# Performance work log

Measured on AMD Instinct MI355X. Metric: run time of the kernel, lower is better.

## Reference

```python
import jax, jax.numpy as jnp
import numpy as np

DIM = 512
HEADS = 8
DIM_HEAD = 64  # default dim_head used for scale, matches DIM//HEADS here
SCALE = DIM_HEAD ** -0.5
B, X, Y = 8, 32, 32


def setup_inputs() -> dict:
    key = jax.random.key(0)
    k0, k1, k2, k3 = jax.random.split(key, 4)
    fmap = jax.random.normal(k0, (B, DIM, X, Y), dtype=jnp.float32)
    # 1x1 convs as matrices: weight [out, in]
    Wqkvl = jax.random.normal(k1, (4 * DIM, DIM), dtype=jnp.float32) * (DIM ** -0.5)
    Wout = jax.random.normal(k2, (DIM, DIM), dtype=jnp.float32) * (DIM ** -0.5)
    bout = jax.random.normal(k3, (DIM,), dtype=jnp.float32) * 0.01
    return {"fmap": fmap, "Wqkvl": Wqkvl, "Wout": Wout, "bout": bout}


def reference(fmap, Wqkvl, Wout, bout):
    b, c, x, y = fmap.shape
    h, d = HEADS, c // HEADS
    n = x * y
    # 1x1 conv projection to q,k,v,L
    qkvL = jnp.einsum('oc,bcxy->boxy', Wqkvl, fmap)  # [b, 4c, x, y]
    q, k, v, L = jnp.split(qkvL, 4, axis=1)
    # 'b (h d) x y -> b h (x y) d'
    def to_tokens(t):
        return t.reshape(b, h, d, n).transpose(0, 1, 3, 2)
    q, k, v, L = map(to_tokens, (q, k, v, L))
    dots = jnp.einsum('bhid,bhjd->bhij', q, k) * SCALE  # [b,h,n,n]
    attn = jax.nn.softmax(dots, axis=-1)
    out = jnp.einsum('bhij,bhjd->bhid', attn, v) + L  # [b,h,n,d]
    # 'b h (x y) d -> b (h d) x y'
    out = out.transpose(0, 1, 3, 2).reshape(b, c, x, y)
    # output 1x1 conv with bias (dropout=0 -> identity)
    out = jnp.einsum('oc,bcxy->boxy', Wout, out) + bout[None, :, None, None]
    return out
```

## Files before the change

### kernel.cpp

```cpp
#include <hip/hip_runtime.h>

#define Bn 8
#define Cn 512
#define Hn 8
#define Dn 64
#define Nn 1024
#define SCALEQ 0.18033688011112042f

typedef unsigned short u16;
typedef unsigned int u32;
typedef unsigned short u16x8 __attribute__((ext_vector_type(8)));
typedef unsigned short u16x4 __attribute__((ext_vector_type(4)));
typedef unsigned int u32x2 __attribute__((ext_vector_type(2)));
typedef short s16x4 __attribute__((ext_vector_type(4)));
typedef float f32x4 __attribute__((ext_vector_type(4)));
typedef __bf16 bf16x8 __attribute__((ext_vector_type(8)));

__device__ __forceinline__ u16 f2bf(float f){
  unsigned u = __float_as_uint(f);
  u += 0x7fffu + ((u >> 16) & 1u);
  return (u16)(u >> 16);
}
__device__ __forceinline__ float bf2f(u16 h){
  return __uint_as_float(((unsigned)h) << 16);
}
__device__ __forceinline__ f32x4 mfma16(u16x8 a, u16x8 b, f32x4 c){
  return __builtin_amdgcn_mfma_f32_16x16x32_bf16(
      __builtin_bit_cast(bf16x8, a), __builtin_bit_cast(bf16x8, b), c, 0, 0, 0);
}
__device__ __forceinline__ f32x4 mfma16k16(u16x4 a, u32x2 b, f32x4 c){
  return __builtin_amdgcn_mfma_f32_16x16x16bf16_1k(
      __builtin_bit_cast(s16x4, a), __builtin_bit_cast(s16x4, b), c, 0, 0, 0);
}
__device__ __forceinline__ float fexp2(float x){ return __builtin_amdgcn_exp2f(x); }
__device__ __forceinline__ u32 cvtpk(float a, float b){
  u32 r;
  asm("v_cvt_pk_bf16_f32 %0, %1, %2" : "=v"(r) : "v"(a), "v"(b));
  return r;
}

__device__ __forceinline__ void gload16(const u16* src, u16* dst){
  __builtin_amdgcn_global_load_lds(
      (const __attribute__((address_space(1))) unsigned int*)src,
      (__attribute__((address_space(3))) unsigned int*)dst, 16, 0, 0);
}

#define TILE_SYNC(N) do {                                     \
    asm volatile("s_waitcnt vmcnt(" #N ")" ::: "memory");     \
    __builtin_amdgcn_sched_barrier(0);                        \
    __builtin_amdgcn_s_barrier();                             \
    __builtin_amdgcn_sched_barrier(0);                        \
  } while(0)

__global__ __launch_bounds__(256) void k_prep(const float* __restrict__ fmap,
                                              u16* __restrict__ fmapT,
                                              const float* __restrict__ Wqkvl,
                                              const float* __restrict__ Wout,
                                              u16* __restrict__ W1bf, u16* __restrict__ Wobf){
  __shared__ float tile[64][33];
  const int bid = blockIdx.x;
  if (bid < 2048){
    const int n0 = (bid & 31) * 32, c0 = ((bid >> 5) & 7) * 64, b = bid >> 8;
    const int tx = threadIdx.x & 31, ty = threadIdx.x >> 5;
    const float* src = fmap + ((size_t)b * Cn + c0) * Nn + n0;
#pragma unroll
    for (int i = 0; i < 8; i++) tile[ty + 8*i][tx] = src[(size_t)(ty + 8*i) * Nn + tx];
    __syncthreads();
    const int nr = threadIdx.x >> 3;
    const int cj = (threadIdx.x & 7) * 8;
    u16x8 o;
#pragma unroll
    for (int k = 0; k < 8; k++) o[k] = f2bf(tile[cj + k][nr]);
    *reinterpret_cast<u16x8*>(fmapT + ((size_t)b * Nn + n0 + nr) * Cn + c0 + cj) = o;
  } else {
    const int n1 = Cn*Cn, n2 = Cn*Cn/4;
    int i = (bid - 2048) * 256 + threadIdx.x;
    const float* s; u16* d; int j;
    if (i < n1){ s = Wqkvl; d = W1bf; j = i; }
    else { if (i >= n1 + n2) return; s = Wout; d = Wobf; j = i - n1; }
    float4 f = reinterpret_cast<const float4*>(s)[j];
    u16x4 o;
    o[0] = f2bf(f.x); o[1] = f2bf(f.y); o[2] = f2bf(f.z); o[3] = f2bf(f.w);
    reinterpret_cast<u16x4*>(d)[j] = o;
  }
}

__device__ __forceinline__ void stage64(const u16* g, size_t ldg, u16* lbase, int w, int lane){
#pragma unroll
  for (int s = 0; s < 2; s++){
    int row = s*32 + w*8 + (lane>>3);
    gload16(g + (size_t)row*ldg + (((lane&7) ^ (row&7)) * 8), lbase + (s*32 + w*8)*64);
  }
}
__device__ __forceinline__ void stage128x32(const u16* g, size_t ldg, u16* lbase, int w, int lane){
#pragma unroll
  for (int s = 0; s < 2; s++){
    int row = s*64 + w*16 + (lane>>2);
    gload16(g + (size_t)row*ldg + (((lane&3) ^ (row&3)) * 8), lbase + (s*64 + w*16)*32);
  }
}
__device__ __forceinline__ void stage64x32(const u16* g, size_t ldg, u16* lbase, int w, int lane){
  int row = w*16 + (lane>>2);
  gload16(g + (size_t)row*ldg + (((lane&3) ^ (row&3)) * 8), lbase + (w*16)*32);
}

__device__ __forceinline__ void gemm_nt_128(const u16* __restrict__ Ap, int lda,
                                            const u16* __restrict__ Bp, int ldb,
                                            u16* sA, u16* sB,
                                            f32x4 (&acc)[4][4]){
  const int tid = threadIdx.x;
  const int w = tid >> 6, lane = tid & 63, r = lane & 15, g = lane >> 4;
  const int wi = w >> 1, wj = w & 1;
  stage128x32(Ap,      lda, sA,        w, lane);
  stage128x32(Bp,      ldb, sB,        w, lane);
  stage128x32(Ap + 32, lda, sA + 4096, w, lane);
  stage128x32(Bp + 32, ldb, sB + 4096, w, lane);
  int cur = 0;
  for (int ks = 0; ks < 16; ks++){
    if (ks < 15) TILE_SYNC(4);
    else         TILE_SYNC(0);
    if (ks + 2 < 16){
      int nxt = cur + 2; if (nxt >= 3) nxt -= 3;
      stage128x32(Ap + (ks+2)*32, lda, sA + nxt*4096, w, lane);
      stage128x32(Bp + (ks+2)*32, ldb, sB + nxt*4096, w, lane);
    }
    const u16* Al = sA + cur*4096;
    const u16* Bl = sB + cur*4096;
    u16x8 af[4], bf[4];
#pragma unroll
    for (int t = 0; t < 4; t++){
      int ar = wi*64 + t*16 + r;
      af[t] = *reinterpret_cast<const u16x8*>(&Al[ar*32 + ((g ^ (ar&3)) * 8)]);
      int br = wj*64 + t*16 + r;
      bf[t] = *reinterpret_cast<const u16x8*>(&Bl[br*32 + ((g ^ (br&3)) * 8)]);
    }
#pragma unroll
    for (int i = 0; i < 4; i++)
#pragma unroll
      for (int j = 0; j < 4; j++)
        acc[i][j] = mfma16(af[i], bf[j], acc[i][j]);
    cur = (cur == 2) ? 0 : cur + 1;
  }
}

__global__ __launch_bounds__(256) void k_gemm1(const u16* __restrict__ fmapT,
                                               const u16* __restrict__ W1,
                                               u16* __restrict__ Qb, u16* __restrict__ Kb,
                                               u16* __restrict__ Vt, u16* __restrict__ Lb){
  __shared__ u16 sA[3*128*32], sB[3*128*32];
  const int lin = blockIdx.x;
  const int wid = (lin & 7) * 128 + (lin >> 3);
  const int ob = wid & 15, nb = (wid >> 4) & 7, b = wid >> 7;
  const int w = threadIdx.x >> 6, wi = w >> 1, wj = w & 1;
  const int lane = threadIdx.x & 63, r = lane & 15, g = lane >> 4;
  const int seg = ob >> 2;

  f32x4 acc[4][4];
  const f32x4 z = {0.f, 0.f, 0.f, 0.f};
#pragma unroll
  for (int i = 0; i < 4; i++)
#pragma unroll
    for (int j = 0; j < 4; j++) acc[i][j] = z;

  const u16* fbase = fmapT + (size_t)b * Nn * Cn;

  if (seg != 2){
    gemm_nt_128(fbase + (size_t)(nb*128) * Cn, Cn, W1 + (size_t)(ob*128) * Cn, Cn, sA, sB, acc);
    u16* dst = (seg == 0) ? Qb : (seg == 1 ? Kb : Lb);
    const float sc = (seg == 0) ? SCALEQ : 1.0f;
#pragma unroll
    for (int it = 0; it < 4; it++)
#pragma unroll
      for (int jt = 0; jt < 4; jt++)
#pragma unroll
        for (int rr = 0; rr < 4; rr++){
          int n = nb*128 + wi*64 + it*16 + 4*g + rr;
          int o = ob*128 + wj*64 + jt*16 + r;
          dst[((size_t)b * Nn + n) * Cn + (o & 511)] = f2bf(acc[it][jt][rr] * sc);
        }
  } else {
    gemm_nt_128(W1 + (size_t)(ob*128) * Cn, Cn, fbase + (size_t)(nb*128) * Cn, Cn, sA, sB, acc);
#pragma unroll
    for (int it = 0; it < 4; it++)
#pragma unroll
      for (int jt = 0; jt < 4; jt++)
#pragma unroll
        for (int rr = 0; rr < 4; rr++){
          int o = ob*128 + wi*64 + it*16 + 4*g + rr;
          int oo = o - 1024;
          int h = oo >> 6, d = oo & 63;
          int n = nb*128 + wj*64 + jt*16 + r;
          Vt[(((size_t)b * Hn + h) * Dn + d) * Nn + n] = f2bf(acc[it][jt][rr]);
        }
  }
}

__global__ __launch_bounds__(256, 4) void k_attn(const u16* __restrict__ Qb,
                                                 const u16* __restrict__ Kb,
                                                 const u16* __restrict__ Vt,
                                                 const u16* __restrict__ Lb,
                                                 u16* __restrict__ tok){
  __shared__ u16 Kl[3*64*64], Vl[3*64*64];
  const int bid = blockIdx.x;
  const int w0 = (bid & 7) * 64 + (bid >> 3);
  const int qblk = w0 & 7, h = (w0 >> 3) & 7, b = w0 >> 6;
  const int w = threadIdx.x >> 6, lane = threadIdx.x & 63;
  const int r = lane & 15, g = lane >> 4;
  const int qA = qblk * 128 + w * 16;
  const int qB = qA + 64;

  const u16* qrowA = Qb + ((size_t)b * Nn + qA + r) * Cn + h * Dn + 8 * g;
  const u16* qrowB = Qb + ((size_t)b * Nn + qB + r) * Cn + h * Dn + 8 * g;
  u16x8 qA0 = *reinterpret_cast<const u16x8*>(qrowA);
  u16x8 qA1 = *reinterpret_cast<const u16x8*>(qrowA + 32);
  u16x8 qB0 = *reinterpret_cast<const u16x8*>(qrowB);
  u16x8 qB1 = *reinterpret_cast<const u16x8*>(qrowB + 32);

  const u16* kbase = Kb + (size_t)b * Nn * Cn + h * Dn;
  const u16* vbase = Vt + ((size_t)b * Hn + h) * Dn * Nn;

  const int koff0 = r*64 + ((g     ^ (r&7)) * 8);
  const int koff1 = r*64 + (((4+g) ^ (r&7)) * 8);
  int voff[4];
#pragma unroll
  for (int s = 0; s < 4; s++)
    voff[s] = r*64 + (((2*s + (g>>1)) ^ (r&7)) * 8) + (g&1)*4;

  f32x4 accA[4], accB[4];
  const f32x4 z = {0.f, 0.f, 0.f, 0.f};
#pragma unroll
  for (int dt = 0; dt < 4; dt++){ accA[dt] = z; accB[dt] = z; }
  f32x4 accSA = z, accSB = z;

  stage64(kbase,         Cn, Kl,        w, lane);
  stage64(vbase,         Nn, Vl,        w, lane);
  stage64(kbase + 64*Cn, Cn, Kl + 4096, w, lane);
  stage64(vbase + 64,    Nn, Vl + 4096, w, lane);

  int cur = 0;
  for (int tile = 0; tile < 16; tile++){
    if (tile < 15) TILE_SYNC(4);
    else           TILE_SYNC(0);
    if (tile + 2 < 16){
      int nxt = cur + 2; if (nxt >= 3) nxt -= 3;
      stage64(kbase + (size_t)(tile+2)*64*Cn, Cn, Kl + nxt*4096, w, lane);
      stage64(vbase + (tile+2)*64,            Nn, Vl + nxt*4096, w, lane);
    }
    const u16* kp0 = Kl + cur*4096 + koff0;
    const u16* kp1 = Kl + cur*4096 + koff1;
    const u16* vp0 = Vl + cur*4096 + voff[0];
    const u16* vp1 = Vl + cur*4096 + voff[1];
    const u16* vp2 = Vl + cur*4096 + voff[2];
    const u16* vp3 = Vl + cur*4096 + voff[3];

    f32x4 sA[4], sB[4];
    __builtin_amdgcn_s_setprio(1);
#pragma unroll
    for (int t = 0; t < 4; t++){
      u16x8 k0 = *reinterpret_cast<const u16x8*>(kp0 + t*1024);
      u16x8 k1 = *reinterpret_cast<const u16x8*>(kp1 + t*1024);
      sA[t] = mfma16(k0, qA0, z); sA[t] = mfma16(k1, qA1, sA[t]);
      sB[t] = mfma16(k0, qB0, z); sB[t] = mfma16(k1, qB1, sB[t]);
    }
    __builtin_amdgcn_s_setprio(0);
    u32x2 pA[4], pB[4];
#pragma unroll
    for (int t = 0; t < 4; t++){
      pA[t][0] = cvtpk(fexp2(sA[t][0]), fexp2(sA[t][1]));
      pA[t][1] = cvtpk(fexp2(sA[t][2]), fexp2(sA[t][3]));
      pB[t][0] = cvtpk(fexp2(sB[t][0]), fexp2(sB[t][1]));
      pB[t][1] = cvtpk(fexp2(sB[t][2]), fexp2(sB[t][3]));
    }
    const u32x2 ones = {0x3F803F80u, 0x3F803F80u};
    __builtin_amdgcn_s_setprio(1);
#pragma unroll
    for (int t = 0; t < 4; t++){
      accSA = mfma16k16(ones[0] == 0 ? u16x4{} : *(const u16x4*)&ones, pA[t], accSA);
      accSB = mfma16k16(*(const u16x4*)&ones, pB[t], accSB);
    }
#pragma unroll
    for (int s = 0; s < 4; s++){
      const u16* vp = (s == 0) ? vp0 : (s == 1) ? vp1 : (s == 2) ? vp2 : vp3;
#pragma unroll
      for (int dt = 0; dt < 4; dt++){
        u16x4 vf = *reinterpret_cast<const u16x4*>(vp + dt*1024);
        accA[dt] = mfma16k16(vf, pA[s], accA[dt]);
        accB[dt] = mfma16k16(vf, pB[s], accB[dt]);
      }
    }
    __builtin_amdgcn_s_setprio(0);
    cur = (cur == 2) ? 0 : cur + 1;
  }

  float linvA = 1.0f / accSA[0];
  float linvB = 1.0f / accSB[0];
#pragma unroll
  for (int half = 0; half < 2; half++){
    const int n = (half ? qB : qA) + r;
    const float linv = half ? linvB : linvA;
    const f32x4* acc = half ? accB : accA;
    const u16* lrow = Lb + ((size_t)b * Nn + n) * Cn + h * Dn;
    u16* trow = tok + ((size_t)b * Nn + n) * Cn + h * Dn;
#pragma unroll
    for (int dt = 0; dt < 4; dt++){
      u16x4 lv = *reinterpret_cast<const u16x4*>(lrow + dt*16 + 4*g);
      u16x4 ov;
#pragma unroll
      for (int rr = 0; rr < 4; rr++)
        ov[rr] = f2bf(acc[dt][rr] * linv + bf2f(lv[rr]));
      *reinterpret_cast<u16x4*>(trow + dt*16 + 4*g) = ov;
    }
  }
}

__global__ __launch_bounds__(256) void k_gemm2(const u16* __restrict__ tok,
                                               const u16* __restrict__ Wo,
                                               const float* __restrict__ bout,
                                               float* __restrict__ out){
  __shared__ u16 sA[3*64*32], sB[3*128*32];
  const int lin = blockIdx.x;
  const int wid = (lin & 7) * 64 + (lin >> 3);
  const int ob = wid & 7, nb = (wid >> 3) & 7, b = wid >> 6;
  const int w = threadIdx.x >> 6, wi = w >> 1, wj = w & 1;
  const int lane = threadIdx.x & 63, r = lane & 15, g = lane >> 4;

  f32x4 acc[2][4];
  const f32x4 z = {0.f, 0.f, 0.f, 0.f};
#pragma unroll
  for (int i = 0; i < 2; i++)
#pragma unroll
    for (int j = 0; j < 4; j++) acc[i][j] = z;

  const u16* Ap = Wo + (size_t)(ob*64) * Cn;
  const u16* Bp = tok + (size_t)b * Nn * Cn + (size_t)(nb*128) * Cn;

  stage64x32 (Ap,      Cn, sA,        w, lane);
  stage128x32(Bp,      Cn, sB,        w, lane);
  stage64x32 (Ap + 32, Cn, sA + 2048, w, lane);
  stage128x32(Bp + 32, Cn, sB + 4096, w, lane);
  int cur = 0;
  for (int ks = 0; ks < 16; ks++){
    if (ks < 15) TILE_SYNC(3);
    else         TILE_SYNC(0);
    if (ks + 2 < 16){
      int nxt = cur + 2; if (nxt >= 3) nxt -= 3;
      stage64x32 (Ap + (ks+2)*32, Cn, sA + nxt*2048, w, lane);
      stage128x32(Bp + (ks+2)*32, Cn, sB + nxt*4096, w, lane);
    }
    const u16* Al = sA + cur*2048;
    const u16* Bl = sB + cur*4096;
    u16x8 af[2], bf[4];
#pragma unroll
    for (int t = 0; t < 2; t++){
      int ar = wi*32 + t*16 + r;
      af[t] = *reinterpret_cast<const u16x8*>(&Al[ar*32 + ((g ^ (ar&3)) * 8)]);
    }
#pragma unroll
    for (int t = 0; t < 4; t++){
      int br = wj*64 + t*16 + r;
      bf[t] = *reinterpret_cast<const u16x8*>(&Bl[br*32 + ((g ^ (br&3)) * 8)]);
    }
#pragma unroll
    for (int i = 0; i < 2; i++)
#pragma unroll
      for (int j = 0; j < 4; j++)
        acc[i][j] = mfma16(af[i], bf[j], acc[i][j]);
    cur = (cur == 2) ? 0 : cur + 1;
  }

#pragma unroll
  for (int it = 0; it < 2; it++)
#pragma unroll
    for (int jt = 0; jt < 4; jt++)
#pragma unroll
      for (int rr = 0; rr < 4; rr++){
        int o = ob*64 + wi*32 + it*16 + 4*g + rr;
        int n = nb*128 + wj*64 + jt*16 + r;
        out[((size_t)b * Cn + o) * Nn + n] = acc[it][jt][rr] + bout[o];
      }
}

extern "C" void kernel_launch(void* const* d_in, const int* in_sizes, int n_in,
                              void* d_out, int out_size, void* d_ws, size_t ws_size,
                              hipStream_t stream){
  const float* fmap  = (const float*)d_in[0];
  const float* Wqkvl = (const float*)d_in[1];
  const float* Wout  = (const float*)d_in[2];
  const float* bout  = (const float*)d_in[3];
  float* out = (float*)d_out;

  char* ws = (char*)d_ws;
  size_t off = 0;
  auto alloc = [&](size_t bytes) -> void* {
    void* p = ws + off;
    off += (bytes + 255) & ~(size_t)255;
    return p;
  };
  u16* W1bf  = (u16*)alloc((size_t)4*Cn*Cn*2);
  u16* Wobf  = (u16*)alloc((size_t)Cn*Cn*2);
  u16* fmapT = (u16*)alloc((size_t)Bn*Nn*Cn*2);
  u16* Qb    = (u16*)alloc((size_t)Bn*Nn*Cn*2);
  u16* Kb    = (u16*)alloc((size_t)Bn*Nn*Cn*2);
  u16* Lb    = (u16*)alloc((size_t)Bn*Nn*Cn*2);
  u16* Vt    = (u16*)alloc((size_t)Bn*Hn*Dn*Nn*2);
  u16* tok   = fmapT;

  hipLaunchKernelGGL(k_prep, dim3(2048 + 1280), dim3(256), 0, stream,
                     fmap, fmapT, Wqkvl, Wout, W1bf, Wobf);
  hipLaunchKernelGGL(k_gemm1, dim3(1024), dim3(256), 0, stream, fmapT, W1bf, Qb, Kb, Vt, Lb);
  hipLaunchKernelGGL(k_attn, dim3(512), dim3(256), 0, stream, Qb, Kb, Vt, Lb, tok);
  hipLaunchKernelGGL(k_gemm2, dim3(512), dim3(256), 0, stream, tok, Wobf, bout, out);
}
```

Measured before the change: 82.36 us.

## Pre-pack K and V into fragment layout and load directly from global in attention

The QKV projection epilogue now writes K and V in a per-head layout that matches the MFMA fragments, so the attention kernel can read K and V fragments straight from global memory (L2-cached) instead of staging them through LDS with a triple-buffered pipeline and barriers. All blocks now use the same GEMM orientation, and k_attn's occupancy hint drops from 4 to 2 to leave room for the extra registers holding prefetched fragments. This removes LDS traffic and block syncs in exchange for repeated global/L2 reads, since every query block rereads the same K/V. It also gives up the explicit prefetch-ahead overlap, and the scattered 2-byte K stores in the GEMM epilogue may be slow.

```diff
diff --git a/kernel.cpp b/kernel.cpp
--- a/kernel.cpp
+++ b/kernel.cpp
@@ -85,13 +85,6 @@
   }
 }
 
-__device__ __forceinline__ void stage64(const u16* g, size_t ldg, u16* lbase, int w, int lane){
-#pragma unroll
-  for (int s = 0; s < 2; s++){
-    int row = s*32 + w*8 + (lane>>3);
-    gload16(g + (size_t)row*ldg + (((lane&7) ^ (row&7)) * 8), lbase + (s*32 + w*8)*64);
-  }
-}
 __device__ __forceinline__ void stage128x32(const u16* g, size_t ldg, u16* lbase, int w, int lane){
 #pragma unroll
   for (int s = 0; s < 2; s++){
@@ -145,8 +138,8 @@
 
 __global__ __launch_bounds__(256) void k_gemm1(const u16* __restrict__ fmapT,
                                                const u16* __restrict__ W1,
-                                               u16* __restrict__ Qb, u16* __restrict__ Kb,
-                                               u16* __restrict__ Vt, u16* __restrict__ Lb){
+                                               u16* __restrict__ Qb, u16* __restrict__ Kp,
+                                               u16* __restrict__ Vp, u16* __restrict__ Lb){
   __shared__ u16 sA[3*128*32], sB[3*128*32];
   const int lin = blockIdx.x;
   const int wid = (lin & 7) * 128 + (lin >> 3);
@@ -163,10 +156,10 @@
     for (int j = 0; j < 4; j++) acc[i][j] = z;
 
   const u16* fbase = fmapT + (size_t)b * Nn * Cn;
-
-  if (seg != 2){
-    gemm_nt_128(fbase + (size_t)(nb*128) * Cn, Cn, W1 + (size_t)(ob*128) * Cn, Cn, sA, sB, acc);
-    u16* dst = (seg == 0) ? Qb : (seg == 1 ? Kb : Lb);
+  gemm_nt_128(fbase + (size_t)(nb*128) * Cn, Cn, W1 + (size_t)(ob*128) * Cn, Cn, sA, sB, acc);
+
+  if (seg == 0 || seg == 3){
+    u16* dst = (seg == 0) ? Qb : Lb;
     const float sc = (seg == 0) ? SCALEQ : 1.0f;
 #pragma unroll
     for (int it = 0; it < 4; it++)
@@ -178,29 +171,42 @@
           int o = ob*128 + wj*64 + jt*16 + r;
           dst[((size_t)b * Nn + n) * Cn + (o & 511)] = f2bf(acc[it][jt][rr] * sc);
         }
+  } else if (seg == 1){
+#pragma unroll
+    for (int it = 0; it < 4; it++)
+#pragma unroll
+      for (int jt = 0; jt < 4; jt++)
+#pragma unroll
+        for (int rr = 0; rr < 4; rr++){
+          int n = nb*128 + wi*64 + it*16 + 4*g + rr;
+          int o = ob*128 + wj*64 + jt*16 + r;
+          int oo = o - 512, hh = oo >> 6, d = oo & 63;
+          size_t off = ((size_t)(b*Hn + hh)*64 + (n>>4))*1024 + (d>>3)*128 + (n&15)*8 + (d&7);
+          Kp[off] = f2bf(acc[it][jt][rr]);
+        }
   } else {
-    gemm_nt_128(W1 + (size_t)(ob*128) * Cn, Cn, fbase + (size_t)(nb*128) * Cn, Cn, sA, sB, acc);
 #pragma unroll
     for (int it = 0; it < 4; it++)
 #pragma unroll
-      for (int jt = 0; jt < 4; jt++)
-#pragma unroll
-        for (int rr = 0; rr < 4; rr++){
-          int o = ob*128 + wi*64 + it*16 + 4*g + rr;
-          int oo = o - 1024;
-          int h = oo >> 6, d = oo & 63;
-          int n = nb*128 + wj*64 + jt*16 + r;
-          Vt[(((size_t)b * Hn + h) * Dn + d) * Nn + n] = f2bf(acc[it][jt][rr]);
-        }
-  }
-}
-
-__global__ __launch_bounds__(256, 4) void k_attn(const u16* __restrict__ Qb,
-                                                 const u16* __restrict__ Kb,
-                                                 const u16* __restrict__ Vt,
+      for (int jt = 0; jt < 4; jt++){
+        int n0 = nb*128 + wi*64 + it*16 + 4*g;
+        int o = ob*128 + wj*64 + jt*16 + r;
+        int oo = o - 1024, hh = oo >> 6, d = oo & 63;
+        u16x4 pk;
+#pragma unroll
+        for (int rr = 0; rr < 4; rr++) pk[rr] = f2bf(acc[it][jt][rr]);
+        size_t off = ((size_t)(b*Hn + hh)*16 + (n0>>6))*4096
+                   + ((n0>>4)&3)*1024 + (d>>4)*256 + ((n0>>2)&3)*64 + (d&15)*4;
+        *reinterpret_cast<u16x4*>(Vp + off) = pk;
+      }
+  }
+}
+
+__global__ __launch_bounds__(256, 2) void k_attn(const u16* __restrict__ Qb,
+                                                 const u16* __restrict__ Kp,
+                                                 const u16* __restrict__ Vp,
                                                  const u16* __restrict__ Lb,
                                                  u16* __restrict__ tok){
-  __shared__ u16 Kl[3*64*64], Vl[3*64*64];
   const int bid = blockIdx.x;
   const int w0 = (bid & 7) * 64 + (bid >> 3);
   const int qblk = w0 & 7, h = (w0 >> 3) & 7, b = w0 >> 6;
@@ -216,15 +222,8 @@
   u16x8 qB0 = *reinterpret_cast<const u16x8*>(qrowB);
   u16x8 qB1 = *reinterpret_cast<const u16x8*>(qrowB + 32);
 
-  const u16* kbase = Kb + (size_t)b * Nn * Cn + h * Dn;
-  const u16* vbase = Vt + ((size_t)b * Hn + h) * Dn * Nn;
-
-  const int koff0 = r*64 + ((g     ^ (r&7)) * 8);
-  const int koff1 = r*64 + (((4+g) ^ (r&7)) * 8);
-  int voff[4];
-#pragma unroll
-  for (int s = 0; s < 4; s++)
-    voff[s] = r*64 + (((2*s + (g>>1)) ^ (r&7)) * 8) + (g&1)*4;
+  const u16* kbase = Kp + (size_t)(b*Hn + h) * 65536 + lane * 8;
+  const u16* vbase = Vp + (size_t)(b*Hn + h) * 65536 + lane * 4;
 
   f32x4 accA[4], accB[4];
   const f32x4 z = {0.f, 0.f, 0.f, 0.f};
@@ -232,37 +231,28 @@
   for (int dt = 0; dt < 4; dt++){ accA[dt] = z; accB[dt] = z; }
   f32x4 accSA = z, accSB = z;
 
-  stage64(kbase,         Cn, Kl,        w, lane);
-  stage64(vbase,         Nn, Vl,        w, lane);
-  stage64(kbase + 64*Cn, Cn, Kl + 4096, w, lane);
-  stage64(vbase + 64,    Nn, Vl + 4096, w, lane);
-
-  int cur = 0;
   for (int tile = 0; tile < 16; tile++){
-    if (tile < 15) TILE_SYNC(4);
-    else           TILE_SYNC(0);
-    if (tile + 2 < 16){
-      int nxt = cur + 2; if (nxt >= 3) nxt -= 3;
-      stage64(kbase + (size_t)(tile+2)*64*Cn, Cn, Kl + nxt*4096, w, lane);
-      stage64(vbase + (tile+2)*64,            Nn, Vl + nxt*4096, w, lane);
-    }
-    const u16* kp0 = Kl + cur*4096 + koff0;
-    const u16* kp1 = Kl + cur*4096 + koff1;
-    const u16* vp0 = Vl + cur*4096 + voff[0];
-    const u16* vp1 = Vl + cur*4096 + voff[1];
-    const u16* vp2 = Vl + cur*4096 + voff[2];
-    const u16* vp3 = Vl + cur*4096 + voff[3];
+    const u16* kt = kbase + tile * 4096;
+    const u16* vt = vbase + tile * 4096;
+    u16x8 k0[4], k1[4];
+#pragma unroll
+    for (int tt = 0; tt < 4; tt++){
+      k0[tt] = *reinterpret_cast<const u16x8*>(kt + tt*1024);
+      k1[tt] = *reinterpret_cast<const u16x8*>(kt + tt*1024 + 512);
+    }
+    u16x4 vf[16];
+#pragma unroll
+    for (int s = 0; s < 4; s++)
+#pragma unroll
+      for (int dt = 0; dt < 4; dt++)
+        vf[s*4+dt] = *reinterpret_cast<const u16x4*>(vt + s*1024 + dt*256);
 
     f32x4 sA[4], sB[4];
-    __builtin_amdgcn_s_setprio(1);
-#pragma unroll
-    for (int t = 0; t < 4; t++){
-      u16x8 k0 = *reinterpret_cast<const u16x8*>(kp0 + t*1024);
-      u16x8 k1 = *reinterpret_cast<const u16x8*>(kp1 + t*1024);
-      sA[t] = mfma16(k0, qA0, z); sA[t] = mfma16(k1, qA1, sA[t]);
-      sB[t] = mfma16(k0, qB0, z); sB[t] = mfma16(k1, qB1, sB[t]);
-    }
-    __builtin_amdgcn_s_setprio(0);
+#pragma unroll
+    for (int tt = 0; tt < 4; tt++){
+      sA[tt] = mfma16(k0[tt], qA0, z); sA[tt] = mfma16(k1[tt], qA1, sA[tt]);
+      sB[tt] = mfma16(k0[tt], qB0, z); sB[tt] = mfma16(k1[tt], qB1, sB[tt]);
+    }
     u32x2 pA[4], pB[4];
 #pragma unroll
     for (int t = 0; t < 4; t++){
@@ -271,25 +261,21 @@
       pB[t][0] = cvtpk(fexp2(sB[t][0]), fexp2(sB[t][1]));
       pB[t][1] = cvtpk(fexp2(sB[t][2]), fexp2(sB[t][3]));
     }
-    const u32x2 ones = {0x3F803F80u, 0x3F803F80u};
-    __builtin_amdgcn_s_setprio(1);
+    const u16x4 ones4 = {0x3F80u, 0x3F80u, 0x3F80u, 0x3F80u};
+    const u32x2 onesw = {0x3F803F80u, 0x3F803F80u};
 #pragma unroll
     for (int t = 0; t < 4; t++){
-      accSA = mfma16k16(ones[0] == 0 ? u16x4{} : *(const u16x4*)&ones, pA[t], accSA);
-      accSB = mfma16k16(*(const u16x4*)&ones, pB[t], accSB);
-    }
-#pragma unroll
-    for (int s = 0; s < 4; s++){
-      const u16* vp = (s == 0) ? vp0 : (s == 1) ? vp1 : (s == 2) ? vp2 : vp3;
+      accSA = mfma16k16(ones4, pA[t], accSA);
+      accSB = mfma16k16(ones4, pB[t], accSB);
+    }
+    (void)onesw;
+#pragma unroll
+    for (int s = 0; s < 4; s++)
 #pragma unroll
       for (int dt = 0; dt < 4; dt++){
-        u16x4 vf = *reinterpret_cast<const u16x4*>(vp + dt*1024);
-        accA[dt] = mfma16k16(vf, pA[s], accA[dt]);
-        accB[dt] = mfma16k16(vf, pB[s], accB[dt]);
+        accA[dt] = mfma16k16(vf[s*4+dt], pA[s], accA[dt]);
+        accB[dt] = mfma16k16(vf[s*4+dt], pB[s], accB[dt]);
       }
-    }
-    __builtin_amdgcn_s_setprio(0);
-    cur = (cur == 2) ? 0 : cur + 1;
   }
 
   float linvA = 1.0f / accSA[0];
@@ -400,14 +386,14 @@
   u16* Wobf  = (u16*)alloc((size_t)Cn*Cn*2);
   u16* fmapT = (u16*)alloc((size_t)Bn*Nn*Cn*2);
   u16* Qb    = (u16*)alloc((size_t)Bn*Nn*Cn*2);
-  u16* Kb    = (u16*)alloc((size_t)Bn*Nn*Cn*2);
+  u16* Kp    = (u16*)alloc((size_t)Bn*Hn*Nn*Dn*2);
   u16* Lb    = (u16*)alloc((size_t)Bn*Nn*Cn*2);
-  u16* Vt    = (u16*)alloc((size_t)Bn*Hn*Dn*Nn*2);
+  u16* Vp    = (u16*)alloc((size_t)Bn*Hn*Dn*Nn*2);
   u16* tok   = fmapT;
 
   hipLaunchKernelGGL(k_prep, dim3(2048 + 1280), dim3(256), 0, stream,
                      fmap, fmapT, Wqkvl, Wout, W1bf, Wobf);
-  hipLaunchKernelGGL(k_gemm1, dim3(1024), dim3(256), 0, stream, fmapT, W1bf, Qb, Kb, Vt, Lb);
-  hipLaunchKernelGGL(k_attn, dim3(512), dim3(256), 0, stream, Qb, Kb, Vt, Lb, tok);
+  hipLaunchKernelGGL(k_gemm1, dim3(1024), dim3(256), 0, stream, fmapT, W1bf, Qb, Kp, Vp, Lb);
+  hipLaunchKernelGGL(k_attn, dim3(512), dim3(256), 0, stream, Qb, Kp, Vp, Lb, tok);
   hipLaunchKernelGGL(k_gemm2, dim3(512), dim3(256), 0, stream, tok, Wobf, bout, out);
 }
```

Result: slower. 85.11 us (+3.3%).
